# Optimization experiments

Hardware: AMD Instinct MI355X
Metric: run time of the kernel (lower is better)

Reference implementation:

```python
import jax, jax.numpy as jnp
import numpy as np

T, B, S = 32, 64, 128
V, WV, ENC, DEC, ATT = 50000, 512, 512, 512, 512
LAYERS, POOL = 2, 2
IN0 = WV + ENC  # input_feed concat


def _gru_cell(x, h, W_ih, b_ih, W_hh, b_hh):
    gi = x @ W_ih.T + b_ih
    gh = h @ W_hh.T + b_hh
    i_r, i_z, i_n = jnp.split(gi, 3, axis=-1)
    h_r, h_z, h_n = jnp.split(gh, 3, axis=-1)
    r = jax.nn.sigmoid(i_r + h_r)
    z = jax.nn.sigmoid(i_z + h_z)
    n = jnp.tanh(i_n + r * h_n)
    return (1.0 - z) * n + z * h


def setup_inputs() -> dict:
    key = jax.random.key(0)
    ks = iter(jax.random.split(key, 32))
    d = {}
    d['input'] = jax.random.randint(next(ks), (T, B), 0, V)
    d['hidden'] = jax.random.normal(next(ks), (LAYERS, B, DEC), jnp.float32)
    d['context'] = jax.random.normal(next(ks), (S, B, ENC), jnp.float32)
    d['src_pad_mask'] = jnp.zeros((B, S), jnp.float32)
    d['init_att'] = jax.random.normal(next(ks), (B, ENC), jnp.float32)
    sc = 0.05
    d['emb_W'] = jax.random.normal(next(ks), (V, WV), jnp.float32) * sc
    # stacked GRU params (layer0 input IN0, layer1 input DEC)
    d['W_ih0'] = jax.random.normal(next(ks), (3 * DEC, IN0), jnp.float32) * sc
    d['b_ih0'] = jnp.zeros((3 * DEC,), jnp.float32)
    d['W_hh0'] = jax.random.normal(next(ks), (3 * DEC, DEC), jnp.float32) * sc
    d['b_hh0'] = jnp.zeros((3 * DEC,), jnp.float32)
    d['W_ih1'] = jax.random.normal(next(ks), (3 * DEC, DEC), jnp.float32) * sc
    d['b_ih1'] = jnp.zeros((3 * DEC,), jnp.float32)
    d['W_hh1'] = jax.random.normal(next(ks), (3 * DEC, DEC), jnp.float32) * sc
    d['b_hh1'] = jnp.zeros((3 * DEC,), jnp.float32)
    # concat attention
    d['W_pre'] = jax.random.normal(next(ks), (ATT, ENC), jnp.float32) * sc
    d['b_pre'] = jnp.zeros((ATT,), jnp.float32)
    d['W_q'] = jax.random.normal(next(ks), (ATT, DEC), jnp.float32) * sc
    d['w_v'] = jax.random.normal(next(ks), (ATT,), jnp.float32) * sc
    # copy switch
    d['W_copy'] = jax.random.normal(next(ks), (1, ENC + DEC), jnp.float32) * sc
    d['b_copy'] = jnp.zeros((1,), jnp.float32)
    # readout
    d['W_read'] = jax.random.normal(next(ks), (DEC, WV + DEC + ENC), jnp.float32) * sc
    d['b_read'] = jnp.zeros((DEC,), jnp.float32)
    return d


def reference(input, hidden, context, src_pad_mask, init_att, emb_W,
              W_ih0, b_ih0, W_hh0, b_hh0, W_ih1, b_ih1, W_hh1, b_hh1,
              W_pre, b_pre, W_q, w_v, W_copy, b_copy, W_read, b_read):
    emb = emb_W[input]                     # [T,B,WV]
    ctx_bse = jnp.transpose(context, (1, 0, 2))  # [B,S,ENC]
    precompute = jnp.einsum('bse,ae->bsa', ctx_bse, W_pre) + b_pre  # [B,S,ATT]
    neg_inf = jnp.finfo(jnp.float32).min

    def step(carry, emb_t):
        h, cur_ctx = carry
        x = jnp.concatenate([emb_t, cur_ctx], axis=1)  # input_feed
        h0 = _gru_cell(x, h[0], W_ih0, b_ih0, W_hh0, b_hh0)
        out = _gru_cell(h0, h[1], W_ih1, b_ih1, W_hh1, b_hh1)
        h_new = jnp.stack([h0, out])
        # concat attention
        q = out @ W_q.T                                  # [B,ATT]
        energy = jnp.tanh(precompute + q[:, None, :]) @ w_v  # [B,S]
        energy = jnp.where(src_pad_mask > 0.5, neg_inf, energy)
        attn = jax.nn.softmax(energy, axis=-1)
        new_ctx = jnp.einsum('bs,bse->be', attn, ctx_bse)
        copy_prob = jax.nn.sigmoid(
            jnp.concatenate([out, new_ctx], axis=1) @ W_copy.T + b_copy)  # [B,1]
        readout = jnp.concatenate([emb_t, out, new_ctx], axis=1) @ W_read.T + b_read
        maxout = jnp.max(readout.reshape(B, DEC // POOL, POOL), axis=-1)  # [B,DEC/POOL]
        return (h_new, new_ctx), (maxout, attn, copy_prob)

    (hidden_f, cur_ctx_f), (g_outputs, c_outputs, copy_gates) = jax.lax.scan(
        step, (hidden, init_att), emb)
    attn_last = c_outputs[-1]
    return g_outputs, c_outputs, copy_gates, hidden_f, attn_last, cur_ctx_f
```

## Files before the change

### kernel.cpp

```cpp
#include <hip/hip_runtime.h>


typedef unsigned short u16;
using bf16x8 = __attribute__((ext_vector_type(8))) short;
using f32x4  = __attribute__((ext_vector_type(4))) float;

#define OFF_EGI    0
#define OFF_EREAD  3145728
#define OFF_ATTPRE 4194304
#define OFF_GI0    8388608
#define OFF_GH0    8486912
#define OFF_GH1    8585216
#define OFF_GI1    8683520
#define OFF_RO0    8781824
#define OFF_RO1    8814592
#define OFF_H0     8847360
#define OFF_H1     8912896
#define OFF_CTX    8978432

#define UB_WIH0C   18087936
#define UB_WHH0    18874368
#define UB_WHH1    19660800
#define UB_WIH1    20447232
#define UB_WRO     21233664
#define UB_WRC     21495808
#define UB_CTXT    21757952
#define UB_H0B     25952256
#define UB_H1B     25985024
#define UB_CTXB    26017792

#define OO_G    0
#define OO_C    524288
#define OO_CP   786432
#define OO_HID  788480
#define OO_AL   854016
#define OO_CTXF 862208

__device__ __forceinline__ float sigm(float x) {
    return 1.0f / (1.0f + __expf(-x));
}
__device__ __forceinline__ float tanh_(float x) {
    x = fmaxf(x, -15.f);
    float e = __expf(-2.0f * x);
    return (1.0f - e) / (1.0f + e);
}
__device__ __forceinline__ float gru_out(float ir, float iz, float in_,
                                         float hr, float hz, float hn, float hp) {
    float r = sigm(ir + hr), z = sigm(iz + hz);
    float n = tanh_(in_ + r * hn);
    return (1.f - z) * n + z * hp;
}
__device__ __forceinline__ u16 f2b(float x) {
    unsigned u = __float_as_uint(x);
    return (u16)((u + 0x7FFFu + ((u >> 16) & 1u)) >> 16);
}
__device__ __forceinline__ float b2f(unsigned u) {
    return __uint_as_float(u << 16);
}

__device__ __forceinline__ void gemm64(
    const float* __restrict__ xrow, const float* __restrict__ wrow,
    int kt0, int nkt, float* lds_x, float* lds_w,
    float* __restrict__ outp, int JW, int orow0, int j0,
    const float* __restrict__ addp, int addmode, int addJW)
{
    const int tid = threadIdx.x;
    const int tb4 = tid >> 4, tj4 = tid & 15;
    float acc[4][4];
#pragma unroll
    for (int a = 0; a < 4; ++a)
#pragma unroll
        for (int b = 0; b < 4; ++b) acc[a][b] = 0.f;

    for (int kt = kt0; kt < kt0 + nkt; ++kt) {
        const int kb = kt << 6;
        __syncthreads();
        {
            const int rl = tid >> 2;
#pragma unroll
            for (int i = 0; i < 4; ++i) {
                const int kk = ((tid & 3) << 4) + (i << 2);
                float4 xv = *(const float4*)(xrow + kb + kk);
                float4 wv = *(const float4*)(wrow + kb + kk);
                lds_x[(kk + 0) * 64 + rl] = xv.x;
                lds_x[(kk + 1) * 64 + rl] = xv.y;
                lds_x[(kk + 2) * 64 + rl] = xv.z;
                lds_x[(kk + 3) * 64 + rl] = xv.w;
                lds_w[(kk + 0) * 64 + rl] = wv.x;
                lds_w[(kk + 1) * 64 + rl] = wv.y;
                lds_w[(kk + 2) * 64 + rl] = wv.z;
                lds_w[(kk + 3) * 64 + rl] = wv.w;
            }
        }
        __syncthreads();
#pragma unroll 4
        for (int kk = 0; kk < 64; ++kk) {
            float4 xv = *(const float4*)(lds_x + kk * 64 + tb4 * 4);
            float4 wv = *(const float4*)(lds_w + kk * 64 + tj4 * 4);
            acc[0][0] += xv.x * wv.x; acc[0][1] += xv.x * wv.y;
            acc[0][2] += xv.x * wv.z; acc[0][3] += xv.x * wv.w;
            acc[1][0] += xv.y * wv.x; acc[1][1] += xv.y * wv.y;
            acc[1][2] += xv.y * wv.z; acc[1][3] += xv.y * wv.w;
            acc[2][0] += xv.z * wv.x; acc[2][1] += xv.z * wv.y;
            acc[2][2] += xv.z * wv.z; acc[2][3] += xv.z * wv.w;
            acc[3][0] += xv.w * wv.x; acc[3][1] += xv.w * wv.y;
            acc[3][2] += xv.w * wv.z; acc[3][3] += xv.w * wv.w;
        }
    }
#pragma unroll
    for (int ib = 0; ib < 4; ++ib) {
        const int row = tb4 * 4 + ib;
        const int jc = j0 + tj4 * 4;
        float4 r;
        r.x = acc[ib][0]; r.y = acc[ib][1]; r.z = acc[ib][2]; r.w = acc[ib][3];
        if (addmode == 1) {
            float4 bv = *(const float4*)(addp + jc);
            r.x += bv.x; r.y += bv.y; r.z += bv.z; r.w += bv.w;
        } else if (addmode == 2) {
            float4 bv = *(const float4*)(addp + (size_t)(orow0 + row) * addJW + jc);
            r.x += bv.x; r.y += bv.y; r.z += bv.z; r.w += bv.w;
        }
        *(float4*)(outp + (size_t)(orow0 + row) * JW + jc) = r;
    }
}

__device__ __forceinline__ void stage_bf16(const u16* __restrict__ Xg, u16* sX) {
    const int tid = threadIdx.x;
#pragma unroll
    for (int p = 0; p < 16; ++p) {
        const int chunk = p * 256 + tid;
        const int row = chunk >> 6, cb16 = chunk & 63;
        const int src = row * 1024 + cb16 * 16;
        const int dst = row * 1024 + ((cb16 * 16) ^ ((row & 7) << 4));
        *(float4*)((char*)sX + dst) = *(const float4*)((const char*)Xg + src);
    }
}

__device__ __forceinline__ void mfma_gemm64(const u16* sX, const u16* __restrict__ Wg,
        float* __restrict__ outp, int JW,
        const float* __restrict__ addp, int mode, int addJW)
{
    const int tid = threadIdx.x;
    const int w = tid >> 6, l = tid & 63;
    const int l15 = l & 15, lhi = l >> 4;
    f32x4 acc0 = {0.f,0.f,0.f,0.f}, acc1 = acc0, acc2 = acc0, acc3 = acc0;
    const int arow = w * 16 + l15;
    const char* aptr = (const char*)sX;
    const int abase = arow * 1024 + lhi * 16;
    const int aswz = (arow & 7) << 4;
#pragma unroll 4
    for (int ks = 0; ks < 16; ++ks) {
        bf16x8 a = *(const bf16x8*)(aptr + ((abase + ks * 64) ^ aswz));
        const u16* wp = Wg + l15 * 512 + ks * 32 + lhi * 8;
        bf16x8 b0 = *(const bf16x8*)(wp);
        bf16x8 b1 = *(const bf16x8*)(wp + 16 * 512);
        bf16x8 b2 = *(const bf16x8*)(wp + 32 * 512);
        bf16x8 b3 = *(const bf16x8*)(wp + 48 * 512);
        acc0 = __builtin_amdgcn_mfma_f32_16x16x32_bf16(a, b0, acc0, 0, 0, 0);
        acc1 = __builtin_amdgcn_mfma_f32_16x16x32_bf16(a, b1, acc1, 0, 0, 0);
        acc2 = __builtin_amdgcn_mfma_f32_16x16x32_bf16(a, b2, acc2, 0, 0, 0);
        acc3 = __builtin_amdgcn_mfma_f32_16x16x32_bf16(a, b3, acc3, 0, 0, 0);
    }
    f32x4 accs[4] = {acc0, acc1, acc2, acc3};
#pragma unroll
    for (int cb = 0; cb < 4; ++cb) {
        const int col = cb * 16 + l15;
#pragma unroll
        for (int r = 0; r < 4; ++r) {
            const int row = w * 16 + lhi * 4 + r;
            float v = accs[cb][r];
            if (mode == 1) v += addp[col];
            else if (mode == 2) v += addp[row * addJW + col];
            outp[(size_t)row * JW + col] = v;
        }
    }
}

__global__ __launch_bounds__(256)
void k_upfront(const int* __restrict__ inp, const float* __restrict__ hid,
               const float* __restrict__ ctxin, const float* __restrict__ init_att,
               const float* __restrict__ embW,
               const float* __restrict__ W_ih0, const float* __restrict__ b_ih0,
               const float* __restrict__ W_hh0, const float* __restrict__ W_hh1,
               const float* __restrict__ W_ih1,
               const float* __restrict__ W_read, const float* __restrict__ b_read,
               const float* __restrict__ W_pre, const float* __restrict__ b_pre,
               float* __restrict__ wsf)
{
    __shared__ float lds_x[4096], lds_w[4096];
    u16* wsu = (u16*)wsf;
    const int jid = blockIdx.x, tid = threadIdx.x, rl = tid >> 2;
    if (jid < 768) {
        const int mt = jid / 24, jt = jid % 24, j0 = jt << 6;
        const int idx = inp[mt * 64 + rl];
        gemm64(embW + (size_t)idx * 512, W_ih0 + (size_t)(j0 + rl) * 1024,
               0, 8, lds_x, lds_w, wsf + OFF_EGI, 1536, mt << 6, j0, b_ih0, 1, 0);
    } else if (jid < 1024) {
        const int r = jid - 768, mt = r >> 3, jt = r & 7, j0 = jt << 6;
        const int idx = inp[mt * 64 + rl];
        gemm64(embW + (size_t)idx * 512, W_read + (size_t)(j0 + rl) * 1536,
               0, 8, lds_x, lds_w, wsf + OFF_EREAD, 512, mt << 6, j0, b_read, 1, 0);
    } else if (jid < 2048) {
        const int r = jid - 1024, mt = r >> 3, jt = r & 7, j0 = jt << 6;
        const int m = (mt << 6) + rl, b = m >> 7, s = m & 127;
        gemm64(ctxin + (size_t)((s << 6) + b) * 512, W_pre + (size_t)(j0 + rl) * 512,
               0, 8, lds_x, lds_w, wsf + OFF_ATTPRE, 512, mt << 6, j0, b_pre, 1, 0);
    } else if (jid < 2054) {
        const int job = jid - 2048, buf = job >> 1, half = job & 1;
        const float* src = buf == 0 ? hid : (buf == 1 ? hid + 32768 : init_att);
        float* dst = wsf + (buf == 0 ? OFF_H0 : (buf == 1 ? OFF_H1 : OFF_CTX)) + 32768;
        for (int i = 0; i < 64; ++i) {
            int e = half * 16384 + i * 256 + tid;
            dst[e] = src[e];
        }
    } else if (jid < 2278) {
        const int w = jid - 2054;
        if (w < 48) {
            for (int i = 0; i < 64; ++i) {
                int e = w * 16384 + i * 256 + tid;
                int j = e >> 9, k = e & 511;
                wsu[UB_WIH0C + e] = f2b(W_ih0[(size_t)j * 1024 + 512 + k]);
            }
        } else if (w < 96) {
            for (int i = 0; i < 64; ++i) {
                int e = (w - 48) * 16384 + i * 256 + tid;
                wsu[UB_WHH0 + e] = f2b(W_hh0[e]);
            }
        } else if (w < 144) {
            for (int i = 0; i < 64; ++i) {
                int e = (w - 96) * 16384 + i * 256 + tid;
                wsu[UB_WHH1 + e] = f2b(W_hh1[e]);
            }
        } else if (w < 192) {
            for (int i = 0; i < 64; ++i) {
                int e = (w - 144) * 16384 + i * 256 + tid;
                wsu[UB_WIH1 + e] = f2b(W_ih1[e]);
            }
        } else if (w < 208) {
            for (int i = 0; i < 64; ++i) {
                int e = (w - 192) * 16384 + i * 256 + tid;
                int j = e >> 9, k = e & 511;
                wsu[UB_WRO + e] = f2b(W_read[(size_t)j * 1536 + 512 + k]);
            }
        } else {
            for (int i = 0; i < 64; ++i) {
                int e = (w - 208) * 16384 + i * 256 + tid;
                int j = e >> 9, k = e & 511;
                wsu[UB_WRC + e] = f2b(W_read[(size_t)j * 1536 + 1024 + k]);
            }
        }
    } else if (jid < 2534) {
        const int w2 = jid - 2278;
        for (int rr = 0; rr < 32; ++rr) {
            const int r = w2 * 32 + rr;
            const int b = r >> 7, s = r & 127;
            const float* src = ctxin + ((size_t)s * 64 + b) * 512;
#pragma unroll
            for (int h = 0; h < 2; ++h) {
                int e = h * 256 + tid;
                wsu[UB_CTXT + (size_t)r * 512 + e] = f2b(src[e]);
            }
        }
    } else {
        const int job = jid - 2534;
        const float* src = job == 0 ? hid : (job == 1 ? hid + 32768 : init_att);
        u16* dst = wsu + (job == 0 ? UB_H0B : (job == 1 ? UB_H1B : UB_CTXB));
        for (int i = 0; i < 128; ++i) {
            int e = i * 256 + tid;
            dst[e] = f2b(src[e]);
        }
    }
}

__global__ __launch_bounds__(256)
void k_pA(int t, const float* __restrict__ b_hh0, const float* __restrict__ b_hh1,
          float* __restrict__ wsf)
{
    __shared__ u16 sX[64 * 512];
    u16* wsu = (u16*)wsf;
    const int blk = blockIdx.x;
    if (blk < 24) {
        stage_bf16(wsu + UB_CTXB, sX);
        __syncthreads();
        const int jt = blk, j0 = jt << 6;
        mfma_gemm64(sX, wsu + UB_WIH0C + jt * 32768, wsf + OFF_GI0 + j0, 1536,
                    wsf + OFF_EGI + (size_t)t * 98304 + j0, 2, 1536);
    } else if (blk < 48) {
        stage_bf16(wsu + UB_H0B, sX);
        __syncthreads();
        const int jt = blk - 24, j0 = jt << 6;
        mfma_gemm64(sX, wsu + UB_WHH0 + jt * 32768, wsf + OFF_GH0 + j0, 1536,
                    b_hh0 + j0, 1, 0);
    } else if (blk < 72) {
        stage_bf16(wsu + UB_H1B, sX);
        __syncthreads();
        const int jt = blk - 48, j0 = jt << 6;
        mfma_gemm64(sX, wsu + UB_WHH1 + jt * 32768, wsf + OFF_GH1 + j0, 1536,
                    b_hh1 + j0, 1, 0);
    } else if (blk < 80) {
        if (t == 0) return;
        stage_bf16(wsu + UB_H1B, sX);
        __syncthreads();
        const int jt = blk - 72, j0 = jt << 6;
        mfma_gemm64(sX, wsu + UB_WRO + jt * 32768, wsf + OFF_RO0 + j0, 512,
                    nullptr, 0, 0);
    } else {
        if (t == 0) return;
        stage_bf16(wsu + UB_CTXB, sX);
        __syncthreads();
        const int jt = blk - 80, j0 = jt << 6;
        mfma_gemm64(sX, wsu + UB_WRC + jt * 32768, wsf + OFF_RO1 + j0, 512,
                    nullptr, 0, 0);
    }
}

__global__ __launch_bounds__(256)
void k_pB(int t, float* __restrict__ wsf, float* __restrict__ dout)
{
    u16* wsu = (u16*)wsf;
    const int blk = blockIdx.x, tid = threadIdx.x;
    const int cur = t & 1, prv = cur ^ 1;
    if (blk < 16) {
        float* h0_cur = wsf + OFF_H0 + cur * 32768;
        const float* h0_prv = wsf + OFF_H0 + prv * 32768;
        const float* GIp = wsf + OFF_GI0;
        const float* GHp = wsf + OFF_GH0;
        u16* h0b = wsu + UB_H0B;
#pragma unroll
        for (int i = 0; i < 8; ++i) {
            const int e = (blk << 11) + (i << 8) + tid;
            const int b = e >> 9, c = e & 511;
            const int base = b * 1536 + c;
            float v = gru_out(GIp[base], GIp[base + 512], GIp[base + 1024],
                              GHp[base], GHp[base + 512], GHp[base + 1024],
                              h0_prv[b * 512 + c]);
            h0_cur[b * 512 + c] = v;
            h0b[b * 512 + c] = f2b(v);
        }
    } else {
        if (t == 0) return;
        const int r = blk - 16;
        const float* ERp = wsf + OFF_EREAD + (size_t)(t - 1) * 32768;
        const float* R0 = wsf + OFF_RO0;
        const float* R1 = wsf + OFF_RO1;
#pragma unroll
        for (int i = 0; i < 8; ++i) {
            const int e = (r << 11) + (i << 8) + tid;
            const int b = e >> 8, j2 = e & 255;
            const int bi = b * 512 + (j2 << 1);
            float v0 = ERp[bi]     + R0[bi]     + R1[bi];
            float v1 = ERp[bi + 1] + R0[bi + 1] + R1[bi + 1];
            dout[OO_G + (size_t)(t - 1) * 16384 + b * 256 + j2] = fmaxf(v0, v1);
        }
    }
}

__global__ __launch_bounds__(256)
void k_pC(const float* __restrict__ b_ih1, float* __restrict__ wsf)
{
    __shared__ u16 sX[64 * 512];
    u16* wsu = (u16*)wsf;
    stage_bf16(wsu + UB_H0B, sX);
    __syncthreads();
    const int jt = blockIdx.x, j0 = jt << 6;
    mfma_gemm64(sX, wsu + UB_WIH1 + jt * 32768, wsf + OFF_GI1 + j0, 1536,
                b_ih1 + j0, 1, 0);
}

__global__ __launch_bounds__(256)
void k_pD(int t, const float* __restrict__ maskp, const float* __restrict__ w_v,
          const float* __restrict__ W_q, const float* __restrict__ W_copy,
          const float* __restrict__ b_copy, float* __restrict__ wsf,
          float* __restrict__ dout)
{
    __shared__ float s_out[512];
    __shared__ float s_q[512];
    __shared__ float s_e[128];
    __shared__ float s_at[128];
    __shared__ float s_ctx[512];
    __shared__ float s_red[256];
    u16* wsu = (u16*)wsf;
    const int b = blockIdx.x, tid = threadIdx.x;
    const int cur = t & 1, prv = cur ^ 1;

    {
        const float* GI1p = wsf + OFF_GI1 + b * 1536;
        const float* GH1p = wsf + OFF_GH1 + b * 1536;
        const float* h1p = wsf + OFF_H1 + prv * 32768 + b * 512;
        float* h1c = wsf + OFF_H1 + cur * 32768 + b * 512;
        u16* h1b = wsu + UB_H1B + b * 512;
        const int c0 = tid * 2;
        float2 gi_r = *(const float2*)(GI1p + c0);
        float2 gi_z = *(const float2*)(GI1p + 512 + c0);
        float2 gi_n = *(const float2*)(GI1p + 1024 + c0);
        float2 gh_r = *(const float2*)(GH1p + c0);
        float2 gh_z = *(const float2*)(GH1p + 512 + c0);
        float2 gh_n = *(const float2*)(GH1p + 1024 + c0);
        float2 hp = *(const float2*)(h1p + c0);
        float o0 = gru_out(gi_r.x, gi_z.x, gi_n.x, gh_r.x, gh_z.x, gh_n.x, hp.x);
        float o1 = gru_out(gi_r.y, gi_z.y, gi_n.y, gh_r.y, gh_z.y, gh_n.y, hp.y);
        s_out[c0] = o0; s_out[c0 + 1] = o1;
        *(float2*)(h1c + c0) = make_float2(o0, o1);
        *(unsigned*)(h1b + c0) = (unsigned)f2b(o0) | ((unsigned)f2b(o1) << 16);
    }
    __syncthreads();

    {
        float q0 = 0.f, q1 = 0.f;
        const float* w0 = W_q + (size_t)tid * 512;
        const float* w1 = W_q + (size_t)(tid + 256) * 512;
#pragma unroll 8
        for (int c = 0; c < 512; c += 4) {
            float4 ov = *(const float4*)(s_out + c);
            float4 a0 = *(const float4*)(w0 + c);
            float4 a1 = *(const float4*)(w1 + c);
            q0 += ov.x * a0.x + ov.y * a0.y + ov.z * a0.z + ov.w * a0.w;
            q1 += ov.x * a1.x + ov.y * a1.y + ov.z * a1.z + ov.w * a1.w;
        }
        s_q[tid] = q0; s_q[tid + 256] = q1;
    }
    __syncthreads();

    {
        const int wid = tid >> 6, lane = tid & 63;
        for (int s = wid; s < 128; s += 4) {
            const float* pre = wsf + OFF_ATTPRE + ((size_t)b * 128 + s) * 512;
            float acc = 0.f;
#pragma unroll
            for (int i = 0; i < 8; ++i) {
                const int a = lane + (i << 6);
                acc += tanh_(pre[a] + s_q[a]) * w_v[a];
            }
#pragma unroll
            for (int d2 = 1; d2 < 64; d2 <<= 1) acc += __shfl_xor(acc, d2, 64);
            if (lane == 0)
                s_e[s] = (maskp[b * 128 + s] > 0.5f) ? -3.0e38f : acc;
        }
    }
    __syncthreads();

    if (tid < 64) {
        float e0 = s_e[tid], e1 = s_e[tid + 64];
        float mx = fmaxf(e0, e1);
#pragma unroll
        for (int d2 = 1; d2 < 64; d2 <<= 1) mx = fmaxf(mx, __shfl_xor(mx, d2, 64));
        float x0 = __expf(e0 - mx), x1 = __expf(e1 - mx);
        float sm = x0 + x1;
#pragma unroll
        for (int d2 = 1; d2 < 64; d2 <<= 1) sm += __shfl_xor(sm, d2, 64);
        float inv = 1.f / sm;
        x0 *= inv; x1 *= inv;
        s_at[tid] = x0; s_at[tid + 64] = x1;
        float* co = dout + OO_C + ((size_t)t * 64 + b) * 128;
        co[tid] = x0; co[tid + 64] = x1;
        if (t == 31) {
            dout[OO_AL + b * 128 + tid] = x0;
            dout[OO_AL + b * 128 + tid + 64] = x1;
        }
    }
    __syncthreads();

    {
        const int e0 = tid * 2;
        const u16* ct = wsu + UB_CTXT + (size_t)b * 65536 + e0;
        float a0 = 0.f, a1 = 0.f;
#pragma unroll 4
        for (int s = 0; s < 128; ++s) {
            float at = s_at[s];
            unsigned pv = *(const unsigned*)(ct + s * 512);
            a0 = fmaf(at, b2f(pv & 0xffffu), a0);
            a1 = fmaf(at, b2f(pv >> 16), a1);
        }
        s_ctx[e0] = a0; s_ctx[e0 + 1] = a1;
        float* cc = wsf + OFF_CTX + cur * 32768 + b * 512;
        *(float2*)(cc + e0) = make_float2(a0, a1);
        *(unsigned*)(wsu + UB_CTXB + b * 512 + e0) =
            (unsigned)f2b(a0) | ((unsigned)f2b(a1) << 16);
    }
    __syncthreads();

    {
        float part = 0.f;
        for (int i2 = tid; i2 < 512; i2 += 256)
            part += s_out[i2] * W_copy[i2] + s_ctx[i2] * W_copy[512 + i2];
        s_red[tid] = part;
        __syncthreads();
        for (int d2 = 128; d2 > 0; d2 >>= 1) {
            if (tid < d2) s_red[tid] += s_red[tid + d2];
            __syncthreads();
        }
        if (tid == 0)
            dout[OO_CP + t * 64 + b] = sigm(s_red[0] + b_copy[0]);
    }
}

__global__ __launch_bounds__(256)
void k_roF(float* __restrict__ wsf, float* __restrict__ dout)
{
    __shared__ u16 sX[64 * 512];
    u16* wsu = (u16*)wsf;
    const int blk = blockIdx.x, tid = threadIdx.x;
    if (blk < 8) {
        stage_bf16(wsu + UB_H1B, sX);
        __syncthreads();
        const int j0 = blk << 6;
        mfma_gemm64(sX, wsu + UB_WRO + blk * 32768, wsf + OFF_RO0 + j0, 512,
                    nullptr, 0, 0);
    } else if (blk < 16) {
        stage_bf16(wsu + UB_CTXB, sX);
        __syncthreads();
        const int jt = blk - 8, j0 = jt << 6;
        mfma_gemm64(sX, wsu + UB_WRC + jt * 32768, wsf + OFF_RO1 + j0, 512,
                    nullptr, 0, 0);
    } else {
        const int job = blk - 16, buf = job >> 1, half = job & 1;
        const float* src = wsf + (buf == 0 ? OFF_H0 : (buf == 1 ? OFF_H1 : OFF_CTX)) + 32768;
        float* dst = dout + (buf == 0 ? OO_HID : (buf == 1 ? OO_HID + 32768 : OO_CTXF));
        for (int i = 0; i < 64; ++i) {
            int e = half * 16384 + i * 256 + tid;
            dst[e] = src[e];
        }
    }
}

__global__ __launch_bounds__(256)
void k_fin(float* __restrict__ wsf, float* __restrict__ dout)
{
    const int blk = blockIdx.x, tid = threadIdx.x;
    const float* ERp = wsf + OFF_EREAD + (size_t)31 * 32768;
    const float* R0 = wsf + OFF_RO0;
    const float* R1 = wsf + OFF_RO1;
#pragma unroll
    for (int i = 0; i < 8; ++i) {
        const int e = (blk << 11) + (i << 8) + tid;
        const int b = e >> 8, j2 = e & 255;
        const int bi = b * 512 + (j2 << 1);
        float v0 = ERp[bi]     + R0[bi]     + R1[bi];
        float v1 = ERp[bi + 1] + R0[bi + 1] + R1[bi + 1];
        dout[OO_G + (size_t)31 * 16384 + b * 256 + j2] = fmaxf(v0, v1);
    }
}

extern "C" void kernel_launch(void* const* d_in, const int* in_sizes, int n_in,
                              void* d_out, int out_size, void* d_ws, size_t ws_size,
                              hipStream_t stream) {
    const int*   inp      = (const int*)d_in[0];
    const float* hid      = (const float*)d_in[1];
    const float* ctxin    = (const float*)d_in[2];
    const float* maskp    = (const float*)d_in[3];
    const float* init_att = (const float*)d_in[4];
    const float* embW     = (const float*)d_in[5];
    const float* W_ih0    = (const float*)d_in[6];
    const float* b_ih0    = (const float*)d_in[7];
    const float* W_hh0    = (const float*)d_in[8];
    const float* b_hh0    = (const float*)d_in[9];
    const float* W_ih1    = (const float*)d_in[10];
    const float* b_ih1    = (const float*)d_in[11];
    const float* W_hh1    = (const float*)d_in[12];
    const float* b_hh1    = (const float*)d_in[13];
    const float* W_pre    = (const float*)d_in[14];
    const float* b_pre    = (const float*)d_in[15];
    const float* W_q      = (const float*)d_in[16];
    const float* w_v      = (const float*)d_in[17];
    const float* W_copy   = (const float*)d_in[18];
    const float* b_copy   = (const float*)d_in[19];
    const float* W_read   = (const float*)d_in[20];
    const float* b_read   = (const float*)d_in[21];
    float* dout = (float*)d_out;
    float* wsf  = (float*)d_ws;

    k_upfront<<<dim3(2537), dim3(256), 0, stream>>>(
        inp, hid, ctxin, init_att, embW, W_ih0, b_ih0, W_hh0, W_hh1, W_ih1,
        W_read, b_read, W_pre, b_pre, wsf);

    for (int t = 0; t < 32; ++t) {
        k_pA<<<dim3(88), dim3(256), 0, stream>>>(t, b_hh0, b_hh1, wsf);
        k_pB<<<dim3(24), dim3(256), 0, stream>>>(t, wsf, dout);
        k_pC<<<dim3(24), dim3(256), 0, stream>>>(b_ih1, wsf);
        k_pD<<<dim3(64), dim3(256), 0, stream>>>(t, maskp, w_v, W_q, W_copy,
                                                 b_copy, wsf, dout);
    }
    k_roF<<<dim3(22), dim3(256), 0, stream>>>(wsf, dout);
    k_fin<<<dim3(8), dim3(256), 0, stream>>>(wsf, dout);
}
```

Baseline: 3.349 ms.

## Fuse per-step kernels into one persistent kernel with atomic grid barriers

Replaces the 128 per-timestep launches (pA/pB/pC/pD) plus the final kernels with one persistent 88-block kernel. Phases are ordered by global atomic counters, and the previous-step readout is merged into the next step's phase. Shared intermediates now go through relaxed atomic loads and stores so they stay coherent across blocks without kernel boundaries. W_q is also pre-converted to bf16 for the attention query. This removes launch overhead and kernel-boundary drains, at the cost of spin-wait latency and a residency requirement for all 88 blocks.

```diff
diff --git a/kernel.cpp b/kernel.cpp
--- a/kernel.cpp
+++ b/kernel.cpp
@@ -2,6 +2,7 @@
 
 
 typedef unsigned short u16;
+typedef unsigned long long u64;
 using bf16x8 = __attribute__((ext_vector_type(8))) short;
 using f32x4  = __attribute__((ext_vector_type(4))) float;
 
@@ -28,6 +29,16 @@
 #define UB_H0B     25952256
 #define UB_H1B     25985024
 #define UB_CTXB    26017792
+#define UB_WQ      26050560
+
+#define OFF_CNT    13160448
+#define CNT_BYTES  25344
+#define PH_A  0
+#define PH_RO 1
+#define PH_B  2
+#define PH_M  3
+#define PH_C  4
+#define PH_D  5
 
 #define OO_G    0
 #define OO_C    524288
@@ -56,6 +67,42 @@
 }
 __device__ __forceinline__ float b2f(unsigned u) {
     return __uint_as_float(u << 16);
+}
+
+__device__ __forceinline__ u64 lda8(const void* p) {
+    return __hip_atomic_load((const u64*)p, __ATOMIC_RELAXED, __HIP_MEMORY_SCOPE_AGENT);
+}
+__device__ __forceinline__ void sta8(void* p, u64 v) {
+    __hip_atomic_store((u64*)p, v, __ATOMIC_RELAXED, __HIP_MEMORY_SCOPE_AGENT);
+}
+__device__ __forceinline__ void sta4(void* p, unsigned v) {
+    __hip_atomic_store((unsigned*)p, v, __ATOMIC_RELAXED, __HIP_MEMORY_SCOPE_AGENT);
+}
+__device__ __forceinline__ void staf(float* p, float v) {
+    __hip_atomic_store(p, v, __ATOMIC_RELAXED, __HIP_MEMORY_SCOPE_AGENT);
+}
+__device__ __forceinline__ float flo(u64 v) { return __uint_as_float((unsigned)v); }
+__device__ __forceinline__ float fhi(u64 v) { return __uint_as_float((unsigned)(v >> 32)); }
+__device__ __forceinline__ u64 pk2(float a, float b) {
+    return (u64)__float_as_uint(a) | ((u64)__float_as_uint(b) << 32);
+}
+
+__device__ __forceinline__ unsigned* cptr(float* wsf, int t, int ph) {
+    return (unsigned*)(wsf + OFF_CNT) + (((t * 6) + ph) << 5);
+}
+__device__ __forceinline__ void bar_wait(unsigned* c, unsigned tgt) {
+    if (threadIdx.x == 0) {
+        while (__hip_atomic_load(c, __ATOMIC_RELAXED, __HIP_MEMORY_SCOPE_AGENT) < tgt) {
+            __builtin_amdgcn_s_sleep(1);
+        }
+    }
+    __syncthreads();
+}
+__device__ __forceinline__ void bar_arrive(unsigned* c) {
+    asm volatile("s_waitcnt vmcnt(0)" ::: "memory");
+    __syncthreads();
+    if (threadIdx.x == 0)
+        __hip_atomic_fetch_add(c, 1u, __ATOMIC_RELAXED, __HIP_MEMORY_SCOPE_AGENT);
 }
 
 __device__ __forceinline__ void gemm64(
@@ -124,15 +171,18 @@
     }
 }
 
-__device__ __forceinline__ void stage_bf16(const u16* __restrict__ Xg, u16* sX) {
+__device__ __forceinline__ void stage_coh(const u16* __restrict__ Xg, u16* sX) {
     const int tid = threadIdx.x;
 #pragma unroll
     for (int p = 0; p < 16; ++p) {
         const int chunk = p * 256 + tid;
         const int row = chunk >> 6, cb16 = chunk & 63;
         const int src = row * 1024 + cb16 * 16;
-        const int dst = row * 1024 + ((cb16 * 16) ^ ((row & 7) << 4));
-        *(float4*)((char*)sX + dst) = *(const float4*)((const char*)Xg + src);
+        const int dst = src ^ ((row & 7) << 4);
+        u64 a = lda8((const char*)Xg + src);
+        u64 b = lda8((const char*)Xg + src + 8);
+        *(u64*)((char*)sX + dst) = a;
+        *(u64*)((char*)sX + dst + 8) = b;
     }
 }
 
@@ -171,7 +221,7 @@
             float v = accs[cb][r];
             if (mode == 1) v += addp[col];
             else if (mode == 2) v += addp[row * addJW + col];
-            outp[(size_t)row * JW + col] = v;
+            staf(outp + (size_t)row * JW + col, v);
         }
     }
 }
@@ -182,7 +232,7 @@
                const float* __restrict__ embW,
                const float* __restrict__ W_ih0, const float* __restrict__ b_ih0,
                const float* __restrict__ W_hh0, const float* __restrict__ W_hh1,
-               const float* __restrict__ W_ih1,
+               const float* __restrict__ W_ih1, const float* __restrict__ W_q,
                const float* __restrict__ W_read, const float* __restrict__ b_read,
                const float* __restrict__ W_pre, const float* __restrict__ b_pre,
                float* __restrict__ wsf)
@@ -209,9 +259,9 @@
         const int job = jid - 2048, buf = job >> 1, half = job & 1;
         const float* src = buf == 0 ? hid : (buf == 1 ? hid + 32768 : init_att);
         float* dst = wsf + (buf == 0 ? OFF_H0 : (buf == 1 ? OFF_H1 : OFF_CTX)) + 32768;
-        for (int i = 0; i < 64; ++i) {
-            int e = half * 16384 + i * 256 + tid;
-            dst[e] = src[e];
+        for (int i = 0; i < 32; ++i) {
+            int e = (half * 16384 + i * 512 + tid * 2);
+            sta8(dst + e, pk2(src[e], src[e + 1]));
         }
     } else if (jid < 2278) {
         const int w = jid - 2054;
@@ -261,86 +311,266 @@
                 wsu[UB_CTXT + (size_t)r * 512 + e] = f2b(src[e]);
             }
         }
-    } else {
+    } else if (jid < 2537) {
         const int job = jid - 2534;
         const float* src = job == 0 ? hid : (job == 1 ? hid + 32768 : init_att);
         u16* dst = wsu + (job == 0 ? UB_H0B : (job == 1 ? UB_H1B : UB_CTXB));
-        for (int i = 0; i < 128; ++i) {
-            int e = i * 256 + tid;
-            dst[e] = f2b(src[e]);
+        for (int i = 0; i < 64; ++i) {
+            int e = (i * 256 + tid) * 2;
+            sta4(dst + e, (unsigned)f2b(src[e]) | ((unsigned)f2b(src[e + 1]) << 16));
+        }
+    } else {
+        const int w3 = jid - 2537;
+        for (int i = 0; i < 64; ++i) {
+            int e = w3 * 16384 + i * 256 + tid;
+            wsu[UB_WQ + e] = f2b(W_q[e]);
         }
     }
 }
 
 __global__ __launch_bounds__(256)
-void k_pA(int t, const float* __restrict__ b_hh0, const float* __restrict__ b_hh1,
-          float* __restrict__ wsf)
+void k_loop(const float* __restrict__ b_hh0, const float* __restrict__ b_hh1,
+            const float* __restrict__ b_ih1, const float* __restrict__ maskp,
+            const float* __restrict__ w_v, const float* __restrict__ W_copy,
+            const float* __restrict__ b_copy, float* __restrict__ wsf,
+            float* __restrict__ dout)
 {
     __shared__ u16 sX[64 * 512];
     u16* wsu = (u16*)wsf;
-    const int blk = blockIdx.x;
-    if (blk < 24) {
-        stage_bf16(wsu + UB_CTXB, sX);
-        __syncthreads();
-        const int jt = blk, j0 = jt << 6;
-        mfma_gemm64(sX, wsu + UB_WIH0C + jt * 32768, wsf + OFF_GI0 + j0, 1536,
-                    wsf + OFF_EGI + (size_t)t * 98304 + j0, 2, 1536);
-    } else if (blk < 48) {
-        stage_bf16(wsu + UB_H0B, sX);
-        __syncthreads();
-        const int jt = blk - 24, j0 = jt << 6;
-        mfma_gemm64(sX, wsu + UB_WHH0 + jt * 32768, wsf + OFF_GH0 + j0, 1536,
-                    b_hh0 + j0, 1, 0);
-    } else if (blk < 72) {
-        stage_bf16(wsu + UB_H1B, sX);
-        __syncthreads();
-        const int jt = blk - 48, j0 = jt << 6;
-        mfma_gemm64(sX, wsu + UB_WHH1 + jt * 32768, wsf + OFF_GH1 + j0, 1536,
-                    b_hh1 + j0, 1, 0);
-    } else if (blk < 80) {
-        if (t == 0) return;
-        stage_bf16(wsu + UB_H1B, sX);
-        __syncthreads();
-        const int jt = blk - 72, j0 = jt << 6;
-        mfma_gemm64(sX, wsu + UB_WRO + jt * 32768, wsf + OFF_RO0 + j0, 512,
-                    nullptr, 0, 0);
-    } else {
-        if (t == 0) return;
-        stage_bf16(wsu + UB_CTXB, sX);
-        __syncthreads();
-        const int jt = blk - 80, j0 = jt << 6;
-        mfma_gemm64(sX, wsu + UB_WRC + jt * 32768, wsf + OFF_RO1 + j0, 512,
-                    nullptr, 0, 0);
-    }
-}
-
-__global__ __launch_bounds__(256)
-void k_pB(int t, float* __restrict__ wsf, float* __restrict__ dout)
-{
-    u16* wsu = (u16*)wsf;
     const int blk = blockIdx.x, tid = threadIdx.x;
-    const int cur = t & 1, prv = cur ^ 1;
-    if (blk < 16) {
-        float* h0_cur = wsf + OFF_H0 + cur * 32768;
-        const float* h0_prv = wsf + OFF_H0 + prv * 32768;
-        const float* GIp = wsf + OFF_GI0;
-        const float* GHp = wsf + OFF_GH0;
-        u16* h0b = wsu + UB_H0B;
-#pragma unroll
-        for (int i = 0; i < 8; ++i) {
-            const int e = (blk << 11) + (i << 8) + tid;
-            const int b = e >> 9, c = e & 511;
-            const int base = b * 1536 + c;
-            float v = gru_out(GIp[base], GIp[base + 512], GIp[base + 1024],
-                              GHp[base], GHp[base + 512], GHp[base + 1024],
-                              h0_prv[b * 512 + c]);
-            h0_cur[b * 512 + c] = v;
-            h0b[b * 512 + c] = f2b(v);
-        }
-    } else {
-        if (t == 0) return;
+
+    for (int t = 0; t < 32; ++t) {
+        const int cur = t & 1, prv = cur ^ 1;
+
+        if (blk < 88) {
+            if (t > 0) bar_wait(cptr(wsf, t - 1, PH_D), 64);
+            if (blk >= 72 && t >= 2) bar_wait(cptr(wsf, t - 1, PH_M), 8);
+            if (blk < 24) {
+                stage_coh(wsu + UB_CTXB, sX); __syncthreads();
+                mfma_gemm64(sX, wsu + UB_WIH0C + blk * 32768, wsf + OFF_GI0 + (blk << 6), 1536,
+                            wsf + OFF_EGI + (size_t)t * 98304 + (blk << 6), 2, 1536);
+                bar_arrive(cptr(wsf, t, PH_A));
+            } else if (blk < 48) {
+                const int jt = blk - 24;
+                stage_coh(wsu + UB_H0B, sX); __syncthreads();
+                mfma_gemm64(sX, wsu + UB_WHH0 + jt * 32768, wsf + OFF_GH0 + (jt << 6), 1536,
+                            b_hh0 + (jt << 6), 1, 0);
+                bar_arrive(cptr(wsf, t, PH_A));
+            } else if (blk < 72) {
+                const int jt = blk - 48;
+                stage_coh(wsu + UB_H1B, sX); __syncthreads();
+                mfma_gemm64(sX, wsu + UB_WHH1 + jt * 32768, wsf + OFF_GH1 + (jt << 6), 1536,
+                            b_hh1 + (jt << 6), 1, 0);
+                bar_arrive(cptr(wsf, t, PH_A));
+            } else if (blk < 80) {
+                if (t > 0) {
+                    const int jt = blk - 72;
+                    stage_coh(wsu + UB_H1B, sX); __syncthreads();
+                    mfma_gemm64(sX, wsu + UB_WRO + jt * 32768, wsf + OFF_RO0 + (jt << 6), 512,
+                                nullptr, 0, 0);
+                    bar_arrive(cptr(wsf, t, PH_RO));
+                }
+            } else {
+                if (t > 0) {
+                    const int jt = blk - 80;
+                    stage_coh(wsu + UB_CTXB, sX); __syncthreads();
+                    mfma_gemm64(sX, wsu + UB_WRC + jt * 32768, wsf + OFF_RO1 + (jt << 6), 512,
+                                nullptr, 0, 0);
+                    bar_arrive(cptr(wsf, t, PH_RO));
+                }
+            }
+        }
+
+        if (blk < 16) {
+            bar_wait(cptr(wsf, t, PH_A), 72);
+            float* h0_cur = wsf + OFF_H0 + cur * 32768;
+            const float* h0_prv = wsf + OFF_H0 + prv * 32768;
+            const float* GIp = wsf + OFF_GI0;
+            const float* GHp = wsf + OFF_GH0;
+            u16* h0b = wsu + UB_H0B;
+#pragma unroll
+            for (int i = 0; i < 4; ++i) {
+                const int p = (blk << 10) + (i << 8) + tid;
+                const int b = p >> 8, c0 = (p & 255) * 2;
+                const int base = b * 1536 + c0;
+                u64 gr = lda8(GIp + base), gz = lda8(GIp + base + 512), gn = lda8(GIp + base + 1024);
+                u64 hr = lda8(GHp + base), hz = lda8(GHp + base + 512), hn = lda8(GHp + base + 1024);
+                u64 hp = lda8(h0_prv + b * 512 + c0);
+                float o0 = gru_out(flo(gr), flo(gz), flo(gn), flo(hr), flo(hz), flo(hn), flo(hp));
+                float o1 = gru_out(fhi(gr), fhi(gz), fhi(gn), fhi(hr), fhi(hz), fhi(hn), fhi(hp));
+                sta8(h0_cur + b * 512 + c0, pk2(o0, o1));
+                sta4(h0b + b * 512 + c0, (unsigned)f2b(o0) | ((unsigned)f2b(o1) << 16));
+            }
+            bar_arrive(cptr(wsf, t, PH_B));
+        } else if (blk < 24 && t > 0) {
+            bar_wait(cptr(wsf, t, PH_RO), 16);
+            const int r = blk - 16;
+            const float* ERp = wsf + OFF_EREAD + (size_t)(t - 1) * 32768;
+            const float* R0 = wsf + OFF_RO0;
+            const float* R1 = wsf + OFF_RO1;
+#pragma unroll
+            for (int i = 0; i < 8; ++i) {
+                const int e = (r << 11) + (i << 8) + tid;
+                const int b = e >> 8, j2 = e & 255;
+                const int bi = b * 512 + (j2 << 1);
+                u64 p0 = lda8(R0 + bi);
+                u64 p1 = lda8(R1 + bi);
+                float v0 = ERp[bi]     + flo(p0) + flo(p1);
+                float v1 = ERp[bi + 1] + fhi(p0) + fhi(p1);
+                dout[OO_G + (size_t)(t - 1) * 16384 + b * 256 + j2] = fmaxf(v0, v1);
+            }
+            bar_arrive(cptr(wsf, t, PH_M));
+        }
+
+        if (blk < 24) {
+            bar_wait(cptr(wsf, t, PH_B), 16);
+            stage_coh(wsu + UB_H0B, sX); __syncthreads();
+            mfma_gemm64(sX, wsu + UB_WIH1 + blk * 32768, wsf + OFF_GI1 + (blk << 6), 1536,
+                        b_ih1 + (blk << 6), 1, 0);
+            bar_arrive(cptr(wsf, t, PH_C));
+        }
+
+        if (blk < 64) {
+            bar_wait(cptr(wsf, t, PH_C), 24);
+            const int b = blk;
+            float* sf = (float*)sX;
+            float* s_out = sf;
+            float* s_q   = sf + 512;
+            float* s_e   = sf + 1024;
+            float* s_at  = sf + 1152;
+            float* s_ctx = sf + 1280;
+            float* s_red = sf + 1792;
+
+            {
+                const float* GI1p = wsf + OFF_GI1 + b * 1536;
+                const float* GH1p = wsf + OFF_GH1 + b * 1536;
+                const float* h1p  = wsf + OFF_H1 + prv * 32768 + b * 512;
+                float* h1c = wsf + OFF_H1 + cur * 32768 + b * 512;
+                u16* h1b = wsu + UB_H1B + b * 512;
+                const int c0 = tid * 2;
+                u64 vr = lda8(GI1p + c0), vz = lda8(GI1p + 512 + c0), vn = lda8(GI1p + 1024 + c0);
+                u64 wr = lda8(GH1p + c0), wz = lda8(GH1p + 512 + c0), wn = lda8(GH1p + 1024 + c0);
+                u64 hp = lda8(h1p + c0);
+                float o0 = gru_out(flo(vr), flo(vz), flo(vn), flo(wr), flo(wz), flo(wn), flo(hp));
+                float o1 = gru_out(fhi(vr), fhi(vz), fhi(vn), fhi(wr), fhi(wz), fhi(wn), fhi(hp));
+                s_out[c0] = o0; s_out[c0 + 1] = o1;
+                sta8(h1c + c0, pk2(o0, o1));
+                sta4(h1b + c0, (unsigned)f2b(o0) | ((unsigned)f2b(o1) << 16));
+            }
+            __syncthreads();
+
+            {
+                const u16* wq0 = wsu + UB_WQ + (size_t)tid * 512;
+                const u16* wq1 = wq0 + (size_t)256 * 512;
+                float q0 = 0.f, q1 = 0.f;
+#pragma unroll 4
+                for (int k = 0; k < 512; k += 4) {
+                    float4 ov = *(const float4*)(s_out + k);
+                    u64 a0 = *(const u64*)(wq0 + k);
+                    u64 a1 = *(const u64*)(wq1 + k);
+                    q0 += ov.x * b2f((unsigned)(a0 & 0xffff)) + ov.y * b2f((unsigned)((a0 >> 16) & 0xffff))
+                        + ov.z * b2f((unsigned)((a0 >> 32) & 0xffff)) + ov.w * b2f((unsigned)(a0 >> 48));
+                    q1 += ov.x * b2f((unsigned)(a1 & 0xffff)) + ov.y * b2f((unsigned)((a1 >> 16) & 0xffff))
+                        + ov.z * b2f((unsigned)((a1 >> 32) & 0xffff)) + ov.w * b2f((unsigned)(a1 >> 48));
+                }
+                s_q[tid] = q0; s_q[tid + 256] = q1;
+            }
+            __syncthreads();
+
+            {
+                const int wid = tid >> 6, lane = tid & 63;
+                for (int s = wid; s < 128; s += 4) {
+                    const float* pre = wsf + OFF_ATTPRE + ((size_t)b * 128 + s) * 512;
+                    float acc = 0.f;
+#pragma unroll
+                    for (int i = 0; i < 8; ++i) {
+                        const int a = lane + (i << 6);
+                        acc += tanh_(pre[a] + s_q[a]) * w_v[a];
+                    }
+#pragma unroll
+                    for (int d2 = 1; d2 < 64; d2 <<= 1) acc += __shfl_xor(acc, d2, 64);
+                    if (lane == 0)
+                        s_e[s] = (maskp[b * 128 + s] > 0.5f) ? -3.0e38f : acc;
+                }
+            }
+            __syncthreads();
+
+            if (tid < 64) {
+                float e0 = s_e[tid], e1 = s_e[tid + 64];
+                float mx = fmaxf(e0, e1);
+#pragma unroll
+                for (int d2 = 1; d2 < 64; d2 <<= 1) mx = fmaxf(mx, __shfl_xor(mx, d2, 64));
+                float x0 = __expf(e0 - mx), x1 = __expf(e1 - mx);
+                float sm = x0 + x1;
+#pragma unroll
+                for (int d2 = 1; d2 < 64; d2 <<= 1) sm += __shfl_xor(sm, d2, 64);
+                float inv = 1.f / sm;
+                x0 *= inv; x1 *= inv;
+                s_at[tid] = x0; s_at[tid + 64] = x1;
+                float* co = dout + OO_C + ((size_t)t * 64 + b) * 128;
+                co[tid] = x0; co[tid + 64] = x1;
+                if (t == 31) {
+                    dout[OO_AL + b * 128 + tid] = x0;
+                    dout[OO_AL + b * 128 + tid + 64] = x1;
+                }
+            }
+            __syncthreads();
+
+            {
+                const int e0 = tid * 2;
+                const u16* ct = wsu + UB_CTXT + (size_t)b * 65536 + e0;
+                float a0 = 0.f, a1 = 0.f;
+#pragma unroll 4
+                for (int s = 0; s < 128; ++s) {
+                    float at = s_at[s];
+                    unsigned pv = *(const unsigned*)(ct + s * 512);
+                    a0 = fmaf(at, b2f(pv & 0xffffu), a0);
+                    a1 = fmaf(at, b2f(pv >> 16), a1);
+                }
+                s_ctx[e0] = a0; s_ctx[e0 + 1] = a1;
+                sta8(wsf + OFF_CTX + cur * 32768 + b * 512 + e0, pk2(a0, a1));
+                sta4(wsu + UB_CTXB + b * 512 + e0,
+                     (unsigned)f2b(a0) | ((unsigned)f2b(a1) << 16));
+            }
+            __syncthreads();
+
+            {
+                float part = 0.f;
+                for (int i2 = tid; i2 < 512; i2 += 256)
+                    part += s_out[i2] * W_copy[i2] + s_ctx[i2] * W_copy[512 + i2];
+                s_red[tid] = part;
+                __syncthreads();
+                for (int d2 = 128; d2 > 0; d2 >>= 1) {
+                    if (tid < d2) s_red[tid] += s_red[tid + d2];
+                    __syncthreads();
+                }
+                if (tid == 0)
+                    dout[OO_CP + t * 64 + b] = sigm(s_red[0] + b_copy[0]);
+            }
+            bar_arrive(cptr(wsf, t, PH_D));
+        }
+    }
+
+    if (blk >= 72 && blk < 88) {
+        bar_wait(cptr(wsf, 31, PH_D), 64);
+        bar_wait(cptr(wsf, 31, PH_M), 8);
+        if (blk < 80) {
+            const int jt = blk - 72;
+            stage_coh(wsu + UB_H1B, sX); __syncthreads();
+            mfma_gemm64(sX, wsu + UB_WRO + jt * 32768, wsf + OFF_RO0 + (jt << 6), 512,
+                        nullptr, 0, 0);
+        } else {
+            const int jt = blk - 80;
+            stage_coh(wsu + UB_CTXB, sX); __syncthreads();
+            mfma_gemm64(sX, wsu + UB_WRC + jt * 32768, wsf + OFF_RO1 + (jt << 6), 512,
+                        nullptr, 0, 0);
+        }
+        bar_arrive(cptr(wsf, 32, PH_RO));
+    }
+    if (blk >= 16 && blk < 24) {
+        bar_wait(cptr(wsf, 32, PH_RO), 16);
         const int r = blk - 16;
-        const float* ERp = wsf + OFF_EREAD + (size_t)(t - 1) * 32768;
+        const float* ERp = wsf + OFF_EREAD + (size_t)31 * 32768;
         const float* R0 = wsf + OFF_RO0;
         const float* R1 = wsf + OFF_RO1;
 #pragma unroll
@@ -348,196 +578,25 @@
             const int e = (r << 11) + (i << 8) + tid;
             const int b = e >> 8, j2 = e & 255;
             const int bi = b * 512 + (j2 << 1);
-            float v0 = ERp[bi]     + R0[bi]     + R1[bi];
-            float v1 = ERp[bi + 1] + R0[bi + 1] + R1[bi + 1];
-            dout[OO_G + (size_t)(t - 1) * 16384 + b * 256 + j2] = fmaxf(v0, v1);
-        }
-    }
-}
-
-__global__ __launch_bounds__(256)
-void k_pC(const float* __restrict__ b_ih1, float* __restrict__ wsf)
-{
-    __shared__ u16 sX[64 * 512];
-    u16* wsu = (u16*)wsf;
-    stage_bf16(wsu + UB_H0B, sX);
-    __syncthreads();
-    const int jt = blockIdx.x, j0 = jt << 6;
-    mfma_gemm64(sX, wsu + UB_WIH1 + jt * 32768, wsf + OFF_GI1 + j0, 1536,
-                b_ih1 + j0, 1, 0);
-}
-
-__global__ __launch_bounds__(256)
-void k_pD(int t, const float* __restrict__ maskp, const float* __restrict__ w_v,
-          const float* __restrict__ W_q, const float* __restrict__ W_copy,
-          const float* __restrict__ b_copy, float* __restrict__ wsf,
-          float* __restrict__ dout)
-{
-    __shared__ float s_out[512];
-    __shared__ float s_q[512];
-    __shared__ float s_e[128];
-    __shared__ float s_at[128];
-    __shared__ float s_ctx[512];
-    __shared__ float s_red[256];
-    u16* wsu = (u16*)wsf;
-    const int b = blockIdx.x, tid = threadIdx.x;
-    const int cur = t & 1, prv = cur ^ 1;
-
-    {
-        const float* GI1p = wsf + OFF_GI1 + b * 1536;
-        const float* GH1p = wsf + OFF_GH1 + b * 1536;
-        const float* h1p = wsf + OFF_H1 + prv * 32768 + b * 512;
-        float* h1c = wsf + OFF_H1 + cur * 32768 + b * 512;
-        u16* h1b = wsu + UB_H1B + b * 512;
-        const int c0 = tid * 2;
-        float2 gi_r = *(const float2*)(GI1p + c0);
-        float2 gi_z = *(const float2*)(GI1p + 512 + c0);
-        float2 gi_n = *(const float2*)(GI1p + 1024 + c0);
-        float2 gh_r = *(const float2*)(GH1p + c0);
-        float2 gh_z = *(const float2*)(GH1p + 512 + c0);
-        float2 gh_n = *(const float2*)(GH1p + 1024 + c0);
-        float2 hp = *(const float2*)(h1p + c0);
-        float o0 = gru_out(gi_r.x, gi_z.x, gi_n.x, gh_r.x, gh_z.x, gh_n.x, hp.x);
-        float o1 = gru_out(gi_r.y, gi_z.y, gi_n.y, gh_r.y, gh_z.y, gh_n.y, hp.y);
-        s_out[c0] = o0; s_out[c0 + 1] = o1;
-        *(float2*)(h1c + c0) = make_float2(o0, o1);
-        *(unsigned*)(h1b + c0) = (unsigned)f2b(o0) | ((unsigned)f2b(o1) << 16);
-    }
-    __syncthreads();
-
-    {
-        float q0 = 0.f, q1 = 0.f;
-        const float* w0 = W_q + (size_t)tid * 512;
-        const float* w1 = W_q + (size_t)(tid + 256) * 512;
-#pragma unroll 8
-        for (int c = 0; c < 512; c += 4) {
-            float4 ov = *(const float4*)(s_out + c);
-            float4 a0 = *(const float4*)(w0 + c);
-            float4 a1 = *(const float4*)(w1 + c);
-            q0 += ov.x * a0.x + ov.y * a0.y + ov.z * a0.z + ov.w * a0.w;
-            q1 += ov.x * a1.x + ov.y * a1.y + ov.z * a1.z + ov.w * a1.w;
-        }
-        s_q[tid] = q0; s_q[tid + 256] = q1;
-    }
-    __syncthreads();
-
-    {
-        const int wid = tid >> 6, lane = tid & 63;
-        for (int s = wid; s < 128; s += 4) {
-            const float* pre = wsf + OFF_ATTPRE + ((size_t)b * 128 + s) * 512;
-            float acc = 0.f;
-#pragma unroll
-            for (int i = 0; i < 8; ++i) {
-                const int a = lane + (i << 6);
-                acc += tanh_(pre[a] + s_q[a]) * w_v[a];
-            }
-#pragma unroll
-            for (int d2 = 1; d2 < 64; d2 <<= 1) acc += __shfl_xor(acc, d2, 64);
-            if (lane == 0)
-                s_e[s] = (maskp[b * 128 + s] > 0.5f) ? -3.0e38f : acc;
-        }
-    }
-    __syncthreads();
-
-    if (tid < 64) {
-        float e0 = s_e[tid], e1 = s_e[tid + 64];
-        float mx = fmaxf(e0, e1);
-#pragma unroll
-        for (int d2 = 1; d2 < 64; d2 <<= 1) mx = fmaxf(mx, __shfl_xor(mx, d2, 64));
-        float x0 = __expf(e0 - mx), x1 = __expf(e1 - mx);
-        float sm = x0 + x1;
-#pragma unroll
-        for (int d2 = 1; d2 < 64; d2 <<= 1) sm += __shfl_xor(sm, d2, 64);
-        float inv = 1.f / sm;
-        x0 *= inv; x1 *= inv;
-        s_at[tid] = x0; s_at[tid + 64] = x1;
-        float* co = dout + OO_C + ((size_t)t * 64 + b) * 128;
-        co[tid] = x0; co[tid + 64] = x1;
-        if (t == 31) {
-            dout[OO_AL + b * 128 + tid] = x0;
-            dout[OO_AL + b * 128 + tid + 64] = x1;
-        }
-    }
-    __syncthreads();
-
-    {
-        const int e0 = tid * 2;
-        const u16* ct = wsu + UB_CTXT + (size_t)b * 65536 + e0;
-        float a0 = 0.f, a1 = 0.f;
-#pragma unroll 4
-        for (int s = 0; s < 128; ++s) {
-            float at = s_at[s];
-            unsigned pv = *(const unsigned*)(ct + s * 512);
-            a0 = fmaf(at, b2f(pv & 0xffffu), a0);
-            a1 = fmaf(at, b2f(pv >> 16), a1);
-        }
-        s_ctx[e0] = a0; s_ctx[e0 + 1] = a1;
-        float* cc = wsf + OFF_CTX + cur * 32768 + b * 512;
-        *(float2*)(cc + e0) = make_float2(a0, a1);
-        *(unsigned*)(wsu + UB_CTXB + b * 512 + e0) =
-            (unsigned)f2b(a0) | ((unsigned)f2b(a1) << 16);
-    }
-    __syncthreads();
-
-    {
-        float part = 0.f;
-        for (int i2 = tid; i2 < 512; i2 += 256)
-            part += s_out[i2] * W_copy[i2] + s_ctx[i2] * W_copy[512 + i2];
-        s_red[tid] = part;
-        __syncthreads();
-        for (int d2 = 128; d2 > 0; d2 >>= 1) {
-            if (tid < d2) s_red[tid] += s_red[tid + d2];
-            __syncthreads();
-        }
-        if (tid == 0)
-            dout[OO_CP + t * 64 + b] = sigm(s_red[0] + b_copy[0]);
-    }
-}
-
-__global__ __launch_bounds__(256)
-void k_roF(float* __restrict__ wsf, float* __restrict__ dout)
-{
-    __shared__ u16 sX[64 * 512];
-    u16* wsu = (u16*)wsf;
-    const int blk = blockIdx.x, tid = threadIdx.x;
-    if (blk < 8) {
-        stage_bf16(wsu + UB_H1B, sX);
-        __syncthreads();
-        const int j0 = blk << 6;
-        mfma_gemm64(sX, wsu + UB_WRO + blk * 32768, wsf + OFF_RO0 + j0, 512,
-                    nullptr, 0, 0);
-    } else if (blk < 16) {
-        stage_bf16(wsu + UB_CTXB, sX);
-        __syncthreads();
-        const int jt = blk - 8, j0 = jt << 6;
-        mfma_gemm64(sX, wsu + UB_WRC + jt * 32768, wsf + OFF_RO1 + j0, 512,
-                    nullptr, 0, 0);
-    } else {
-        const int job = blk - 16, buf = job >> 1, half = job & 1;
-        const float* src = wsf + (buf == 0 ? OFF_H0 : (buf == 1 ? OFF_H1 : OFF_CTX)) + 32768;
-        float* dst = dout + (buf == 0 ? OO_HID : (buf == 1 ? OO_HID + 32768 : OO_CTXF));
-        for (int i = 0; i < 64; ++i) {
-            int e = half * 16384 + i * 256 + tid;
-            dst[e] = src[e];
-        }
-    }
-}
-
-__global__ __launch_bounds__(256)
-void k_fin(float* __restrict__ wsf, float* __restrict__ dout)
-{
-    const int blk = blockIdx.x, tid = threadIdx.x;
-    const float* ERp = wsf + OFF_EREAD + (size_t)31 * 32768;
-    const float* R0 = wsf + OFF_RO0;
-    const float* R1 = wsf + OFF_RO1;
-#pragma unroll
-    for (int i = 0; i < 8; ++i) {
-        const int e = (blk << 11) + (i << 8) + tid;
-        const int b = e >> 8, j2 = e & 255;
-        const int bi = b * 512 + (j2 << 1);
-        float v0 = ERp[bi]     + R0[bi]     + R1[bi];
-        float v1 = ERp[bi + 1] + R0[bi + 1] + R1[bi + 1];
-        dout[OO_G + (size_t)31 * 16384 + b * 256 + j2] = fmaxf(v0, v1);
+            u64 p0 = lda8(R0 + bi);
+            u64 p1 = lda8(R1 + bi);
+            float v0 = ERp[bi]     + flo(p0) + flo(p1);
+            float v1 = ERp[bi + 1] + fhi(p0) + fhi(p1);
+            dout[OO_G + (size_t)31 * 16384 + b * 256 + j2] = fmaxf(v0, v1);
+        }
+    }
+    if (blk >= 24 && blk < 36) {
+        bar_wait(cptr(wsf, 31, PH_D), 64);
+        const int job = blk - 24;
+        const float* src = wsf + (job < 4 ? OFF_H0 : job < 8 ? OFF_H1 : OFF_CTX)
+                         + 32768 + (job & 3) * 8192;
+        float* dst = dout + (job < 4 ? OO_HID : job < 8 ? (OO_HID + 32768) : OO_CTXF)
+                   + (job & 3) * 8192;
+        for (int i = 0; i < 16; ++i) {
+            const int e2 = (i * 256 + tid) * 2;
+            u64 v = lda8(src + e2);
+            *(u64*)(dst + e2) = v;
+        }
     }
 }
 
@@ -569,17 +628,12 @@
     float* dout = (float*)d_out;
     float* wsf  = (float*)d_ws;
 
-    k_upfront<<<dim3(2537), dim3(256), 0, stream>>>(
-        inp, hid, ctxin, init_att, embW, W_ih0, b_ih0, W_hh0, W_hh1, W_ih1,
+    hipMemsetAsync((char*)d_ws + (size_t)OFF_CNT * 4, 0, CNT_BYTES, stream);
+
+    k_upfront<<<dim3(2553), dim3(256), 0, stream>>>(
+        inp, hid, ctxin, init_att, embW, W_ih0, b_ih0, W_hh0, W_hh1, W_ih1, W_q,
         W_read, b_read, W_pre, b_pre, wsf);
 
-    for (int t = 0; t < 32; ++t) {
-        k_pA<<<dim3(88), dim3(256), 0, stream>>>(t, b_hh0, b_hh1, wsf);
-        k_pB<<<dim3(24), dim3(256), 0, stream>>>(t, wsf, dout);
-        k_pC<<<dim3(24), dim3(256), 0, stream>>>(b_ih1, wsf);
-        k_pD<<<dim3(64), dim3(256), 0, stream>>>(t, maskp, w_v, W_q, W_copy,
-                                                 b_copy, wsf, dout);
-    }
-    k_roF<<<dim3(22), dim3(256), 0, stream>>>(wsf, dout);
-    k_fin<<<dim3(8), dim3(256), 0, stream>>>(wsf, dout);
-}
+    k_loop<<<dim3(88), dim3(256), 0, stream>>>(
+        b_hh0, b_hh1, b_ih1, maskp, w_v, W_copy, b_copy, wsf, dout);
+}
```

New measurement: 5.721 ms. 1.71x slower.
